# Performance work log

Measured on AMD Instinct MI355X. Metric: run time of the kernel, lower is better.

Reference implementation:

```python
import jax, jax.numpy as jnp
import numpy as np

B, S, D = 2, 2048, 1024
H, DK = 16, 64            # num_heads, d_kv; inner_dim = H*DK = 1024
NUM_BUCKETS = 32
MAX_DISTANCE = 128


def _relative_position_bucket(relative_position, bidirectional=True,
                              num_buckets=NUM_BUCKETS, max_distance=MAX_DISTANCE):
    # Faithful port of Mesh-TF / HF T5 bucketing (int32 in, int32 buckets out).
    relative_buckets = jnp.zeros_like(relative_position)
    if bidirectional:
        num_buckets = num_buckets // 2
        relative_buckets = relative_buckets + (relative_position > 0).astype(jnp.int32) * num_buckets
        relative_position = jnp.abs(relative_position)
    else:
        relative_position = -jnp.minimum(relative_position, 0)
    max_exact = num_buckets // 2
    is_small = relative_position < max_exact
    # log-spaced buckets for large distances; guard log(0) (masked by is_small anyway)
    rel_f = jnp.maximum(relative_position, 1).astype(jnp.float32)
    val_if_large = max_exact + (
        jnp.log(rel_f / max_exact) / np.log(max_distance / max_exact) * (num_buckets - max_exact)
    ).astype(jnp.int32)
    val_if_large = jnp.minimum(val_if_large, num_buckets - 1)
    return relative_buckets + jnp.where(is_small, relative_position, val_if_large)


def compute_bias(rel_emb, query_length, key_length):
    ctx = jnp.arange(query_length, dtype=jnp.int32)[:, None]
    mem = jnp.arange(key_length, dtype=jnp.int32)[None, :]
    buckets = _relative_position_bucket(mem - ctx, bidirectional=True)  # [q, k]
    values = rel_emb[buckets]                       # [q, k, H]
    return jnp.transpose(values, (2, 0, 1))[None]   # [1, H, q, k]


def setup_inputs() -> dict:
    key = jax.random.key(0)
    ks = jax.random.split(key, 6)
    scale = 1.0 / np.sqrt(D)
    return {
        "hidden_states": jax.random.normal(ks[0], (B, S, D), jnp.float32),
        "wq": jax.random.normal(ks[1], (D, H * DK), jnp.float32) * scale,
        "wk": jax.random.normal(ks[2], (D, H * DK), jnp.float32) * scale,
        "wv": jax.random.normal(ks[3], (D, H * DK), jnp.float32) * scale,
        "wo": jax.random.normal(ks[4], (H * DK, D), jnp.float32) * scale,
        "rel_emb": jax.random.normal(ks[5], (NUM_BUCKETS, H), jnp.float32),
    }


def reference(hidden_states, wq, wk, wv, wo, rel_emb):
    b, s, _ = hidden_states.shape

    def shape(x):  # [B,S,H*DK] -> [B,H,S,DK]
        return x.reshape(b, s, H, DK).transpose(0, 2, 1, 3)

    q = shape(hidden_states @ wq)   # NOTE: T5 does not scale q by 1/sqrt(d_kv)
    k = shape(hidden_states @ wk)
    v = shape(hidden_states @ wv)

    scores = jnp.einsum("bhqd,bhkd->bhqk", q, k)
    position_bias = compute_bias(rel_emb, s, s)     # [1,H,S,S]
    scores = scores + position_bias
    attn = jax.nn.softmax(scores, axis=-1)
    ctx = jnp.einsum("bhqk,bhkd->bhqd", attn, v)    # [B,H,S,DK]
    ctx = ctx.transpose(0, 2, 1, 3).reshape(b, s, H * DK)
    return ctx @ wo
```

## Files before the change

### kernel.cpp

```cpp
#include <hip/hip_runtime.h>


typedef __attribute__((ext_vector_type(8)))  unsigned short u16x8;
typedef __attribute__((ext_vector_type(4)))  unsigned short u16x4;
typedef __attribute__((ext_vector_type(8)))  __bf16         bf16x8;
typedef __attribute__((ext_vector_type(4)))  float          f32x4;
typedef __attribute__((ext_vector_type(4)))  unsigned int   u32x4;

#define GLOBAL_AS __attribute__((address_space(1)))
#define LDS_AS    __attribute__((address_space(3)))

static __device__ inline f32x4 MFMA(u16x8 a, u16x8 b, f32x4 c) {
  return __builtin_amdgcn_mfma_f32_16x16x32_bf16(
      __builtin_bit_cast(bf16x8, a), __builtin_bit_cast(bf16x8, b), c, 0, 0, 0);
}

static __device__ inline void gload16(const void* g, void* l) {
  __builtin_amdgcn_global_load_lds((const GLOBAL_AS unsigned int*)g,
                                   (LDS_AS unsigned int*)l, 16, 0, 0);
}

static __device__ inline unsigned short f2bf(float x) {
  unsigned int u = __builtin_bit_cast(unsigned int, x);
  u = (u + 0x7FFFu + ((u >> 16) & 1u)) >> 16;
  return (unsigned short)u;
}

static __device__ inline unsigned int cvtpk(float lo, float hi) {
  unsigned int r;
  asm volatile("v_cvt_pk_bf16_f32 %0, %1, %2" : "=v"(r) : "v"(lo), "v"(hi));
  return r;
}

static __device__ inline float max3f(float a, float b, float c) {
  float r;
  asm volatile("v_max3_f32 %0, %1, %2, %3" : "=v"(r) : "v"(a), "v"(b), "v"(c));
  return r;
}

#define L2E 1.4426950408889634f

__global__ __launch_bounds__(256) void k_prep(const float* __restrict__ hs,
                                              const float* __restrict__ wq,
                                              const float* __restrict__ wk,
                                              const float* __restrict__ wv,
                                              const float* __restrict__ wo,
                                              const float* __restrict__ re,
                                              unsigned short* __restrict__ hsb,
                                              unsigned short* __restrict__ wt,
                                              unsigned short* __restrict__ wot,
                                              float* __restrict__ btab) {
  __shared__ float tile[64][65];
  const int bid = blockIdx.x;
  const int t = threadIdx.x;

  if (bid < 4096) {
    int i = bid * 256 + t;
    float4 v = *(const float4*)(hs + (size_t)i * 4);
    u16x4 o;
    o[0] = f2bf(v.x); o[1] = f2bf(v.y); o[2] = f2bf(v.z); o[3] = f2bf(v.w);
    *(u16x4*)(hsb + (size_t)i * 4) = o;
  } else if (bid < 5120) {
    int sub = bid - 4096;
    int which = sub >> 8;
    int sb = sub & 255;
    int n0 = (sb & 15) << 6, k0 = (sb >> 4) << 6;
    const float* src = which == 0 ? wq : which == 1 ? wk : which == 2 ? wv : wo;
    unsigned short* dst = which == 0 ? wt
                        : which == 1 ? wt + 1048576
                        : which == 2 ? wt + 2097152 : wot;
    const int K = 1024, N = 1024;
    int rr = t >> 4, cc = (t & 15) << 2;
#pragma unroll
    for (int j = 0; j < 4; j++) {
      float4 v = *(const float4*)(src + (size_t)(k0 + rr + j * 16) * N + n0 + cc);
      tile[rr + j * 16][cc + 0] = v.x;
      tile[rr + j * 16][cc + 1] = v.y;
      tile[rr + j * 16][cc + 2] = v.z;
      tile[rr + j * 16][cc + 3] = v.w;
    }
    __syncthreads();
#pragma unroll
    for (int j = 0; j < 4; j++) {
      int n = rr + j * 16;
      u16x4 o;
      o[0] = f2bf(tile[cc + 0][n]);
      o[1] = f2bf(tile[cc + 1][n]);
      o[2] = f2bf(tile[cc + 2][n]);
      o[3] = f2bf(tile[cc + 3][n]);
      *(u16x4*)(dst + (size_t)(n0 + n) * K + k0 + cc) = o;
    }
  } else {
    int i = (bid - 5120) * 256 + t;
    if (i < 16 * 4095) {
      int h = i / 4095;
      int rp = i % 4095 - 2047;
      int rb = rp > 0 ? 16 : 0;
      int arp = rp < 0 ? -rp : rp;
      int v;
      if (arp < 8) {
        v = arp;
      } else {
        float tt = logf((float)arp * 0.125f);
        tt = tt / 2.772588722239781f;
        tt = tt * 8.0f;
        v = 8 + (int)tt;
        if (v > 15) v = 15;
      }
      btab[i] = re[(rb + v) * 16 + h] * L2E;
    }
  }
}

template <int EPI>
__global__ __launch_bounds__(256) void k_gemm(const unsigned short* __restrict__ A,
                                              const unsigned short* __restrict__ Bt,
                                              void* __restrict__ outp,
                                              int M, int N, int K) {
  __shared__ __attribute__((aligned(16))) char smem[32768];
  const int tid = threadIdx.x;
  const int lane = tid & 63, w = tid >> 6;
  const int l15 = lane & 15, g = lane >> 4;
  const int wr = w >> 1, wc = w & 1;
  const int bm0 = blockIdx.y << 7, bn0 = blockIdx.x << 7;

  const char* Ag = (const char*)A + (size_t)bm0 * K * 2;
  const char* Bg = (const char*)Bt + (size_t)bn0 * K * 2;

  f32x4 acc[4][4];
#pragma unroll
  for (int i = 0; i < 4; i++)
#pragma unroll
    for (int j = 0; j < 4; j++) acc[i][j] = (f32x4)0.0f;

  const int rowA = wr * 64 + l15;
  const int rowB = wc * 64 + l15;
  const int swz = (l15 & 7) << 4;

  for (int kt = 0; kt < K; kt += 64) {
#pragma unroll
    for (int j = 0; j < 4; j++) {
      int idx = ((j * 4 + w) << 10) + (lane << 4);
      int row = idx >> 7;
      int gs = (idx >> 4) & 7;
      size_t co = (size_t)row * (K * 2) + kt * 2 + ((gs ^ (row & 7)) << 4);
      gload16(Ag + co, smem + ((j * 4 + w) << 10));
      gload16(Bg + co, smem + 16384 + ((j * 4 + w) << 10));
    }
    __syncthreads();
#pragma unroll
    for (int kk = 0; kk < 2; kk++) {
      const int cp = ((kk << 6) + (g << 4)) ^ swz;
      u16x8 af[4], bfv[4];
#pragma unroll
      for (int mt = 0; mt < 4; mt++)
        af[mt] = *(const u16x8*)(smem + ((rowA + mt * 16) << 7) + cp);
#pragma unroll
      for (int nt = 0; nt < 4; nt++)
        bfv[nt] = *(const u16x8*)(smem + 16384 + ((rowB + nt * 16) << 7) + cp);
#pragma unroll
      for (int mt = 0; mt < 4; mt++)
#pragma unroll
        for (int nt = 0; nt < 4; nt++)
          acc[mt][nt] = MFMA(af[mt], bfv[nt], acc[mt][nt]);
    }
    __syncthreads();
  }

#pragma unroll
  for (int mt = 0; mt < 4; mt++) {
#pragma unroll
    for (int nt = 0; nt < 4; nt++) {
#pragma unroll
      for (int r = 0; r < 4; r++) {
        int m = bm0 + wr * 64 + mt * 16 + g * 4 + r;
        int n = bn0 + wc * 64 + nt * 16 + l15;
        float val = acc[mt][nt][r];
        if (EPI == 0) {
          int which = n >> 10;
          int hh = (n >> 6) & 15;
          int d = n & 63;
          int bb = m >> 11, s = m & 2047;
          int plane = bb * 16 + hh;
          unsigned short* o = (unsigned short*)outp;
          if (which == 0) {
            o[(size_t)plane * 131072 + (size_t)s * 64 + d] = f2bf(val * L2E);
          } else if (which == 1) {
            o[4194304 + (size_t)plane * 131072 + (size_t)s * 64 + d] = f2bf(val);
          } else {
            o[8388608 + (size_t)plane * 131072 + (size_t)d * 2048 + s] = f2bf(val);
          }
        } else {
          ((float*)outp)[(size_t)m * N + n] = val;
        }
      }
    }
  }
}

__global__ __launch_bounds__(512, 6) void k_attn(const unsigned short* __restrict__ qkv,
                                                 const float* __restrict__ btab,
                                                 unsigned short* __restrict__ ctx) {
  __shared__ __attribute__((aligned(16))) char smem[65536];
  const int tid = threadIdx.x;
  const int lane = tid & 63, w = tid >> 6;
  const int l15 = lane & 15, g = lane >> 4;

  const int wg = ((blockIdx.x & 7) << 6) + (blockIdx.x >> 3);
  const int plane = wg >> 4, qb = wg & 15;
  const int h = plane & 15, b = plane >> 4;
  const int q0 = (qb << 7) + (w << 4);

  const unsigned short* Qp = qkv + (size_t)plane * 131072;
  const unsigned short* Kp = qkv + 4194304 + (size_t)plane * 131072;
  const unsigned short* Vt = qkv + 8388608 + (size_t)plane * 131072;

  u16x8 qa[2];
#pragma unroll
  for (int kk = 0; kk < 2; kk++)
    qa[kk] = *(const u16x8*)(Qp + (size_t)(q0 + l15) * 64 + kk * 32 + g * 8);

  float m_r = 0.0f;
  f32x4 oacc[4], lacc;
#pragma unroll
  for (int t = 0; t < 4; t++) oacc[t] = (f32x4)0.0f;
  lacc = (f32x4)0.0f;

  const float* brow = btab + h * 4095 + 2047 - q0;
  const float cpos = btab[h * 4095 + 2047 + 1024];
  const float cneg = btab[h * 4095 + 2047 - 1024];

  u16x8 ones;
  {
    u32x4 ov = {0x3F803F80u, 0x3F803F80u, 0x3F803F80u, 0x3F803F80u};
    ones = __builtin_bit_cast(u16x8, ov);
  }

  const int srow = (w << 3) + (lane >> 3);
  const int soff = ((lane & 7) ^ (srow & 7)) << 4;
  const char* Ksrc = (const char*)Kp + (size_t)srow * 128 + soff;
  const char* Vsrc = (const char*)Vt + (size_t)srow * 4096 + soff;

  auto STAGE = [&](int t, int bsel) {
    char* sb = smem + (bsel << 14) + (w << 10);
    gload16(Ksrc + (size_t)t * 8192, sb);
    gload16(Vsrc + (size_t)t * 128, sb + 8192);
  };

  auto TILE = [&](int t, int bsel) {
    const char* kb = smem + (bsel << 14);
    const char* vbuf = kb + 8192;
    const int kv = t << 6;

    int delta_t = kv - q0;
    bool far = (delta_t >= 112 || delta_t <= -160);
    float cb = far ? (delta_t > 0 ? cpos : cneg) : 0.0f;
    float ebi = cb - m_r;
    f32x4 z0 = {ebi, ebi, ebi, ebi};

    f32x4 s[4];
    __builtin_amdgcn_s_setprio(1);
#pragma unroll
    for (int nt = 0; nt < 4; nt++) {
      int keyr = nt * 16 + l15;
      int sw = (keyr & 7) << 4;
      u16x8 kb0 = *(const u16x8*)(kb + (keyr << 7) + ((g << 4) ^ sw));
      u16x8 kb1 = *(const u16x8*)(kb + (keyr << 7) + ((64 + (g << 4)) ^ sw));
      f32x4 z = MFMA(kb0, qa[0], z0);
      z = MFMA(kb1, qa[1], z);
      s[nt] = z;
    }
    __builtin_amdgcn_s_setprio(0);

    if (!far) {
      const float* bp = brow + kv + (g << 2) - l15;
#pragma unroll
      for (int nt = 0; nt < 4; nt++)
#pragma unroll
        for (int r = 0; r < 4; r++) s[nt][r] += bp[nt * 16 + r];
    }

    float ma = max3f(s[0][0], s[0][1], s[0][2]);
    ma = max3f(ma, s[0][3], s[1][0]);
    ma = max3f(ma, s[1][1], s[1][2]);
    ma = fmaxf(ma, s[1][3]);
    float mb = max3f(s[2][0], s[2][1], s[2][2]);
    mb = max3f(mb, s[2][3], s[3][0]);
    mb = max3f(mb, s[3][1], s[3][2]);
    mb = fmaxf(mb, s[3][3]);
    float mloc = fmaxf(ma, mb);

    if (!__all(mloc <= 12.0f)) {
      float mxrow = fmaxf(mloc, __shfl_xor(mloc, 16));
      mxrow = fmaxf(mxrow, __shfl_xor(mxrow, 32));
      float dlt = fmaxf(mxrow, 0.0f);
      m_r += dlt;
      float alpha = exp2f(-dlt);
#pragma unroll
      for (int nt = 0; nt < 4; nt++)
#pragma unroll
        for (int r = 0; r < 4; r++) s[nt][r] -= dlt;
      float a4[4];
#pragma unroll
      for (int r = 0; r < 4; r++) a4[r] = __shfl(alpha, (g << 2) + r);
#pragma unroll
      for (int tt = 0; tt < 4; tt++) {
        f32x4 o = oacc[tt];
        o[0] *= a4[0]; o[1] *= a4[1]; o[2] *= a4[2]; o[3] *= a4[3];
        oacc[tt] = o;
      }
      lacc[0] *= a4[0]; lacc[1] *= a4[1]; lacc[2] *= a4[2]; lacc[3] *= a4[3];
    }

    unsigned int wpk[4][2];
#pragma unroll
    for (int nt = 0; nt < 4; nt++) {
#pragma unroll
      for (int r = 0; r < 4; r++)
        s[nt][r] = __builtin_amdgcn_exp2f(s[nt][r]);
      wpk[nt][0] = cvtpk(s[nt][0], s[nt][1]);
      wpk[nt][1] = cvtpk(s[nt][2], s[nt][3]);
    }
    u16x8 pa[2];
#pragma unroll
    for (int kk = 0; kk < 2; kk++) {
      unsigned int X0 = wpk[2 * kk][0], Y0 = wpk[2 * kk + 1][0];
      asm volatile("v_permlane32_swap_b32 %0, %1" : "+v"(X0), "+v"(Y0));
      asm volatile("v_permlane16_swap_b32 %0, %1" : "+v"(X0), "+v"(Y0));
      unsigned int X1 = wpk[2 * kk][1], Y1 = wpk[2 * kk + 1][1];
      asm volatile("v_permlane32_swap_b32 %0, %1" : "+v"(X1), "+v"(Y1));
      asm volatile("v_permlane16_swap_b32 %0, %1" : "+v"(X1), "+v"(Y1));
      u32x4 pw = {X0, X1, Y0, Y1};
      pa[kk] = __builtin_bit_cast(u16x8, pw);
    }

    __builtin_amdgcn_s_setprio(1);
#pragma unroll
    for (int tt = 0; tt < 4; tt++) {
      int d = tt * 16 + l15;
      int sw = (d & 7) << 4;
      u16x8 vb0 = *(const u16x8*)(vbuf + (d << 7) + ((g << 4) ^ sw));
      u16x8 vb1 = *(const u16x8*)(vbuf + (d << 7) + ((64 + (g << 4)) ^ sw));
      oacc[tt] = MFMA(pa[0], vb0, oacc[tt]);
      oacc[tt] = MFMA(pa[1], vb1, oacc[tt]);
    }
    lacc = MFMA(pa[0], ones, lacc);
    lacc = MFMA(pa[1], ones, lacc);
    __builtin_amdgcn_s_setprio(0);
  };

  STAGE(0, 0);
  STAGE(1, 1);
  __syncthreads();

  for (int it = 0; it < 16; ++it) {
    const int p  = (it & 1) << 1;
    const int sp = ((it + 1) & 1) << 1;
    if (it < 15) {
      STAGE(2 * it + 2, sp);
      STAGE(2 * it + 3, sp + 1);
    }
    TILE(2 * it, p);
    __builtin_amdgcn_sched_barrier(0);
    TILE(2 * it + 1, p + 1);
    __syncthreads();
  }

#pragma unroll
  for (int r = 0; r < 4; r++) {
    float inv = 1.0f / lacc[r];
    size_t rowoff = ((size_t)(b * 2048 + q0 + (g << 2) + r) << 10) + h * 64;
#pragma unroll
    for (int tt = 0; tt < 4; tt++)
      ctx[rowoff + tt * 16 + l15] = f2bf(oacc[tt][r] * inv);
  }
}

extern "C" void kernel_launch(void* const* d_in, const int* in_sizes, int n_in,
                              void* d_out, int out_size, void* d_ws, size_t ws_size,
                              hipStream_t stream) {
  const float* hs = (const float*)d_in[0];
  const float* wq = (const float*)d_in[1];
  const float* wk = (const float*)d_in[2];
  const float* wv = (const float*)d_in[3];
  const float* wo = (const float*)d_in[4];
  const float* re = (const float*)d_in[5];

  if (ws_size < 50593728u) return;

  char* ws = (char*)d_ws;
  unsigned short* hsb = (unsigned short*)(ws);
  unsigned short* wt  = (unsigned short*)(ws + 8388608);
  unsigned short* wot = (unsigned short*)(ws + 14680064);
  unsigned short* qkv = (unsigned short*)(ws + 16777216);
  unsigned short* ctx = (unsigned short*)(ws + 41943040);
  float*          btab = (float*)(ws + 50331648);

  k_prep<<<5376, 256, 0, stream>>>(hs, wq, wk, wv, wo, re, hsb, wt, wot, btab);
  k_gemm<0><<<dim3(24, 32), 256, 0, stream>>>(hsb, wt, qkv, 4096, 3072, 1024);
  k_attn<<<512, 512, 0, stream>>>(qkv, btab, ctx);
  k_gemm<1><<<dim3(8, 32), 256, 0, stream>>>(ctx, wot, d_out, 4096, 1024, 1024);
}
```

Measured before the change: 121.4 us.

## Process two 16-row query fragments per wave to reuse K/V register fragments

```diff
diff --git a/kernel.cpp b/kernel.cpp
--- a/kernel.cpp
+++ b/kernel.cpp
@@ -198,7 +198,7 @@
   }
 }
 
-__global__ __launch_bounds__(512, 6) void k_attn(const unsigned short* __restrict__ qkv,
+__global__ __launch_bounds__(256, 2) void k_attn(const unsigned short* __restrict__ qkv,
                                                  const float* __restrict__ btab,
                                                  unsigned short* __restrict__ ctx) {
   __shared__ __attribute__((aligned(16))) char smem[65536];
@@ -209,24 +209,27 @@
   const int wg = ((blockIdx.x & 7) << 6) + (blockIdx.x >> 3);
   const int plane = wg >> 4, qb = wg & 15;
   const int h = plane & 15, b = plane >> 4;
-  const int q0 = (qb << 7) + (w << 4);
+  const int q0w = (qb << 7) + (w << 5);
 
   const unsigned short* Qp = qkv + (size_t)plane * 131072;
   const unsigned short* Kp = qkv + 4194304 + (size_t)plane * 131072;
   const unsigned short* Vt = qkv + 8388608 + (size_t)plane * 131072;
 
-  u16x8 qa[2];
-#pragma unroll
-  for (int kk = 0; kk < 2; kk++)
-    qa[kk] = *(const u16x8*)(Qp + (size_t)(q0 + l15) * 64 + kk * 32 + g * 8);
-
-  float m_r = 0.0f;
-  f32x4 oacc[4], lacc;
-#pragma unroll
-  for (int t = 0; t < 4; t++) oacc[t] = (f32x4)0.0f;
-  lacc = (f32x4)0.0f;
-
-  const float* brow = btab + h * 4095 + 2047 - q0;
+  u16x8 qaA[2], qaB[2];
+#pragma unroll
+  for (int kk = 0; kk < 2; kk++) {
+    qaA[kk] = *(const u16x8*)(Qp + (size_t)(q0w + l15) * 64 + kk * 32 + g * 8);
+    qaB[kk] = *(const u16x8*)(Qp + (size_t)(q0w + 16 + l15) * 64 + kk * 32 + g * 8);
+  }
+
+  float m_rA = 0.0f, m_rB = 0.0f;
+  f32x4 oaccA[4], oaccB[4], laccA, laccB;
+#pragma unroll
+  for (int t = 0; t < 4; t++) { oaccA[t] = (f32x4)0.0f; oaccB[t] = (f32x4)0.0f; }
+  laccA = (f32x4)0.0f; laccB = (f32x4)0.0f;
+
+  const float* browA = btab + h * 4095 + 2047 - q0w;
+  const float* browB = browA - 16;
   const float cpos = btab[h * 4095 + 2047 + 1024];
   const float cneg = btab[h * 4095 + 2047 - 1024];
 
@@ -236,15 +239,19 @@
     ones = __builtin_bit_cast(u16x8, ov);
   }
 
-  const int srow = (w << 3) + (lane >> 3);
+  const int srow = (w << 4) + (lane >> 3);
   const int soff = ((lane & 7) ^ (srow & 7)) << 4;
-  const char* Ksrc = (const char*)Kp + (size_t)srow * 128 + soff;
-  const char* Vsrc = (const char*)Vt + (size_t)srow * 4096 + soff;
+  const char* KsrcA = (const char*)Kp + (size_t)srow * 128 + soff;
+  const char* KsrcB = KsrcA + 1024;
+  const char* VsrcA = (const char*)Vt + (size_t)srow * 4096 + soff;
+  const char* VsrcB = VsrcA + 32768;
 
   auto STAGE = [&](int t, int bsel) {
-    char* sb = smem + (bsel << 14) + (w << 10);
-    gload16(Ksrc + (size_t)t * 8192, sb);
-    gload16(Vsrc + (size_t)t * 128, sb + 8192);
+    char* sb = smem + (bsel << 14) + (w << 11);
+    gload16(KsrcA + (size_t)t * 8192, sb);
+    gload16(KsrcB + (size_t)t * 8192, sb + 1024);
+    gload16(VsrcA + (size_t)t * 128, sb + 8192);
+    gload16(VsrcB + (size_t)t * 128, sb + 8192 + 1024);
   };
 
   auto TILE = [&](int t, int bsel) {
@@ -252,101 +259,116 @@
     const char* vbuf = kb + 8192;
     const int kv = t << 6;
 
-    int delta_t = kv - q0;
-    bool far = (delta_t >= 112 || delta_t <= -160);
-    float cb = far ? (delta_t > 0 ? cpos : cneg) : 0.0f;
-    float ebi = cb - m_r;
-    f32x4 z0 = {ebi, ebi, ebi, ebi};
-
-    f32x4 s[4];
-    __builtin_amdgcn_s_setprio(1);
+    u16x8 kf[4][2], vf[4][2];
 #pragma unroll
     for (int nt = 0; nt < 4; nt++) {
       int keyr = nt * 16 + l15;
       int sw = (keyr & 7) << 4;
-      u16x8 kb0 = *(const u16x8*)(kb + (keyr << 7) + ((g << 4) ^ sw));
-      u16x8 kb1 = *(const u16x8*)(kb + (keyr << 7) + ((64 + (g << 4)) ^ sw));
-      f32x4 z = MFMA(kb0, qa[0], z0);
-      z = MFMA(kb1, qa[1], z);
-      s[nt] = z;
-    }
-    __builtin_amdgcn_s_setprio(0);
-
-    if (!far) {
-      const float* bp = brow + kv + (g << 2) - l15;
-#pragma unroll
-      for (int nt = 0; nt < 4; nt++)
-#pragma unroll
-        for (int r = 0; r < 4; r++) s[nt][r] += bp[nt * 16 + r];
-    }
-
-    float ma = max3f(s[0][0], s[0][1], s[0][2]);
-    ma = max3f(ma, s[0][3], s[1][0]);
-    ma = max3f(ma, s[1][1], s[1][2]);
-    ma = fmaxf(ma, s[1][3]);
-    float mb = max3f(s[2][0], s[2][1], s[2][2]);
-    mb = max3f(mb, s[2][3], s[3][0]);
-    mb = max3f(mb, s[3][1], s[3][2]);
-    mb = fmaxf(mb, s[3][3]);
-    float mloc = fmaxf(ma, mb);
-
-    if (!__all(mloc <= 12.0f)) {
-      float mxrow = fmaxf(mloc, __shfl_xor(mloc, 16));
-      mxrow = fmaxf(mxrow, __shfl_xor(mxrow, 32));
-      float dlt = fmaxf(mxrow, 0.0f);
-      m_r += dlt;
-      float alpha = exp2f(-dlt);
-#pragma unroll
-      for (int nt = 0; nt < 4; nt++)
-#pragma unroll
-        for (int r = 0; r < 4; r++) s[nt][r] -= dlt;
-      float a4[4];
-#pragma unroll
-      for (int r = 0; r < 4; r++) a4[r] = __shfl(alpha, (g << 2) + r);
-#pragma unroll
-      for (int tt = 0; tt < 4; tt++) {
-        f32x4 o = oacc[tt];
-        o[0] *= a4[0]; o[1] *= a4[1]; o[2] *= a4[2]; o[3] *= a4[3];
-        oacc[tt] = o;
-      }
-      lacc[0] *= a4[0]; lacc[1] *= a4[1]; lacc[2] *= a4[2]; lacc[3] *= a4[3];
-    }
-
-    unsigned int wpk[4][2];
-#pragma unroll
-    for (int nt = 0; nt < 4; nt++) {
-#pragma unroll
-      for (int r = 0; r < 4; r++)
-        s[nt][r] = __builtin_amdgcn_exp2f(s[nt][r]);
-      wpk[nt][0] = cvtpk(s[nt][0], s[nt][1]);
-      wpk[nt][1] = cvtpk(s[nt][2], s[nt][3]);
-    }
-    u16x8 pa[2];
-#pragma unroll
-    for (int kk = 0; kk < 2; kk++) {
-      unsigned int X0 = wpk[2 * kk][0], Y0 = wpk[2 * kk + 1][0];
-      asm volatile("v_permlane32_swap_b32 %0, %1" : "+v"(X0), "+v"(Y0));
-      asm volatile("v_permlane16_swap_b32 %0, %1" : "+v"(X0), "+v"(Y0));
-      unsigned int X1 = wpk[2 * kk][1], Y1 = wpk[2 * kk + 1][1];
-      asm volatile("v_permlane32_swap_b32 %0, %1" : "+v"(X1), "+v"(Y1));
-      asm volatile("v_permlane16_swap_b32 %0, %1" : "+v"(X1), "+v"(Y1));
-      u32x4 pw = {X0, X1, Y0, Y1};
-      pa[kk] = __builtin_bit_cast(u16x8, pw);
-    }
-
-    __builtin_amdgcn_s_setprio(1);
+      kf[nt][0] = *(const u16x8*)(kb + (keyr << 7) + ((g << 4) ^ sw));
+      kf[nt][1] = *(const u16x8*)(kb + (keyr << 7) + ((64 + (g << 4)) ^ sw));
+    }
 #pragma unroll
     for (int tt = 0; tt < 4; tt++) {
       int d = tt * 16 + l15;
       int sw = (d & 7) << 4;
-      u16x8 vb0 = *(const u16x8*)(vbuf + (d << 7) + ((g << 4) ^ sw));
-      u16x8 vb1 = *(const u16x8*)(vbuf + (d << 7) + ((64 + (g << 4)) ^ sw));
-      oacc[tt] = MFMA(pa[0], vb0, oacc[tt]);
-      oacc[tt] = MFMA(pa[1], vb1, oacc[tt]);
-    }
-    lacc = MFMA(pa[0], ones, lacc);
-    lacc = MFMA(pa[1], ones, lacc);
-    __builtin_amdgcn_s_setprio(0);
+      vf[tt][0] = *(const u16x8*)(vbuf + (d << 7) + ((g << 4) ^ sw));
+      vf[tt][1] = *(const u16x8*)(vbuf + (d << 7) + ((64 + (g << 4)) ^ sw));
+    }
+
+    auto FRAG = [&](const u16x8* qa, float& m_r, f32x4* oacc, f32x4& lacc,
+                    const float* brow, int qf) {
+      int delta_t = kv - qf;
+      bool far = (delta_t >= 112 || delta_t <= -160);
+      float cb = far ? (delta_t > 0 ? cpos : cneg) : 0.0f;
+      float ebi = cb - m_r;
+      f32x4 z0 = {ebi, ebi, ebi, ebi};
+
+      f32x4 s[4];
+      __builtin_amdgcn_s_setprio(1);
+#pragma unroll
+      for (int nt = 0; nt < 4; nt++) {
+        f32x4 z = MFMA(kf[nt][0], qa[0], z0);
+        z = MFMA(kf[nt][1], qa[1], z);
+        s[nt] = z;
+      }
+      __builtin_amdgcn_s_setprio(0);
+
+      if (!far) {
+        const float* bp = brow + kv + (g << 2) - l15;
+#pragma unroll
+        for (int nt = 0; nt < 4; nt++)
+#pragma unroll
+          for (int r = 0; r < 4; r++) s[nt][r] += bp[nt * 16 + r];
+      }
+
+      float ma = max3f(s[0][0], s[0][1], s[0][2]);
+      ma = max3f(ma, s[0][3], s[1][0]);
+      ma = max3f(ma, s[1][1], s[1][2]);
+      ma = fmaxf(ma, s[1][3]);
+      float mb = max3f(s[2][0], s[2][1], s[2][2]);
+      mb = max3f(mb, s[2][3], s[3][0]);
+      mb = max3f(mb, s[3][1], s[3][2]);
+      mb = fmaxf(mb, s[3][3]);
+      float mloc = fmaxf(ma, mb);
+
+      if (!__all(mloc <= 12.0f)) {
+        float mxrow = fmaxf(mloc, __shfl_xor(mloc, 16));
+        mxrow = fmaxf(mxrow, __shfl_xor(mxrow, 32));
+        float dlt = fmaxf(mxrow, 0.0f);
+        m_r += dlt;
+        float alpha = exp2f(-dlt);
+#pragma unroll
+        for (int nt = 0; nt < 4; nt++)
+#pragma unroll
+          for (int r = 0; r < 4; r++) s[nt][r] -= dlt;
+        float a4[4];
+#pragma unroll
+        for (int r = 0; r < 4; r++) a4[r] = __shfl(alpha, (g << 2) + r);
+#pragma unroll
+        for (int tt = 0; tt < 4; tt++) {
+          f32x4 o = oacc[tt];
+          o[0] *= a4[0]; o[1] *= a4[1]; o[2] *= a4[2]; o[3] *= a4[3];
+          oacc[tt] = o;
+        }
+        lacc[0] *= a4[0]; lacc[1] *= a4[1]; lacc[2] *= a4[2]; lacc[3] *= a4[3];
+      }
+
+      unsigned int wpk[4][2];
+#pragma unroll
+      for (int nt = 0; nt < 4; nt++) {
+#pragma unroll
+        for (int r = 0; r < 4; r++)
+          s[nt][r] = __builtin_amdgcn_exp2f(s[nt][r]);
+        wpk[nt][0] = cvtpk(s[nt][0], s[nt][1]);
+        wpk[nt][1] = cvtpk(s[nt][2], s[nt][3]);
+      }
+      u16x8 pa[2];
+#pragma unroll
+      for (int kk = 0; kk < 2; kk++) {
+        unsigned int X0 = wpk[2 * kk][0], Y0 = wpk[2 * kk + 1][0];
+        asm volatile("v_permlane32_swap_b32 %0, %1" : "+v"(X0), "+v"(Y0));
+        asm volatile("v_permlane16_swap_b32 %0, %1" : "+v"(X0), "+v"(Y0));
+        unsigned int X1 = wpk[2 * kk][1], Y1 = wpk[2 * kk + 1][1];
+        asm volatile("v_permlane32_swap_b32 %0, %1" : "+v"(X1), "+v"(Y1));
+        asm volatile("v_permlane16_swap_b32 %0, %1" : "+v"(X1), "+v"(Y1));
+        u32x4 pw = {X0, X1, Y0, Y1};
+        pa[kk] = __builtin_bit_cast(u16x8, pw);
+      }
+
+      __builtin_amdgcn_s_setprio(1);
+#pragma unroll
+      for (int tt = 0; tt < 4; tt++) {
+        oacc[tt] = MFMA(pa[0], vf[tt][0], oacc[tt]);
+        oacc[tt] = MFMA(pa[1], vf[tt][1], oacc[tt]);
+      }
+      lacc = MFMA(pa[0], ones, lacc);
+      lacc = MFMA(pa[1], ones, lacc);
+      __builtin_amdgcn_s_setprio(0);
+    };
+
+    FRAG(qaA, m_rA, oaccA, laccA, browA, q0w);
+    __builtin_amdgcn_sched_barrier(0);
+    FRAG(qaB, m_rB, oaccB, laccB, browB, q0w + 16);
   };
 
   STAGE(0, 0);
@@ -368,11 +390,19 @@
 
 #pragma unroll
   for (int r = 0; r < 4; r++) {
-    float inv = 1.0f / lacc[r];
-    size_t rowoff = ((size_t)(b * 2048 + q0 + (g << 2) + r) << 10) + h * 64;
+    float inv = 1.0f / laccA[r];
+    size_t rowoff = ((size_t)(b * 2048 + q0w + (g << 2) + r) << 10) + h * 64;
 #pragma unroll
     for (int tt = 0; tt < 4; tt++)
-      ctx[rowoff + tt * 16 + l15] = f2bf(oacc[tt][r] * inv);
+      ctx[rowoff + tt * 16 + l15] = f2bf(oaccA[tt][r] * inv);
+  }
+#pragma unroll
+  for (int r = 0; r < 4; r++) {
+    float inv = 1.0f / laccB[r];
+    size_t rowoff = ((size_t)(b * 2048 + q0w + 16 + (g << 2) + r) << 10) + h * 64;
+#pragma unroll
+    for (int tt = 0; tt < 4; tt++)
+      ctx[rowoff + tt * 16 + l15] = f2bf(oaccB[tt][r] * inv);
   }
 }
 
@@ -398,6 +428,6 @@
 
   k_prep<<<5376, 256, 0, stream>>>(hs, wq, wk, wv, wo, re, hsb, wt, wot, btab);
   k_gemm<0><<<dim3(24, 32), 256, 0, stream>>>(hsb, wt, qkv, 4096, 3072, 1024);
-  k_attn<<<512, 512, 0, stream>>>(qkv, btab, ctx);
+  k_attn<<<512, 256, 0, stream>>>(qkv, btab, ctx);
   k_gemm<1><<<dim3(8, 32), 256, 0, stream>>>(ctx, wot, d_out, 4096, 1024, 1024);
 }
```

After: 123.4 us. About the same (+1.7%).
